# Performance work log

Measured on AMD Instinct MI355X. Metric: run time of the kernel, lower is better.

## Reference

```python
import jax, jax.numpy as jnp
import numpy as np

HEADDIM = 128
CHUNK = 256


def _ssd_scan(x, dt, A, B, C, chunk):
    # x: (b,l,h,p)  dt: (b,l,h)  A: (h,)  B,C: (b,l,n)  (single group g=1 shared by all heads)
    b, l, h, p = x.shape
    n = B.shape[-1]
    nc = l // chunk
    dA = dt * A  # (b,l,h)
    xc = x.reshape(b, nc, chunk, h, p)
    dtc = dt.reshape(b, nc, chunk, h)
    dAc = dA.reshape(b, nc, chunk, h)
    Bc = B.reshape(b, nc, chunk, n)
    Cc = C.reshape(b, nc, chunk, n)
    cs = jnp.cumsum(dAc, axis=2)  # (b,nc,c,h) cumulative log-decay within chunk
    # intra-chunk quadratic part
    CB = jnp.einsum('bjin,bjkn->bjik', Cc, Bc)  # (b,nc,c,c)
    decay = jnp.exp(cs[:, :, :, None, :] - cs[:, :, None, :, :])  # (b,nc,i,k,h)
    mask = jnp.tril(jnp.ones((chunk, chunk), dtype=bool))
    decay = jnp.where(mask[None, None, :, :, None], decay, 0.0)
    y_intra = jnp.einsum('bjik,bjikh,bjkh,bjkhp->bjihp', CB, decay, dtc, xc)
    # per-chunk end states
    decay_states = jnp.exp(cs[:, :, -1:, :] - cs)  # (b,nc,c,h)
    states = jnp.einsum('bjkh,bjkh,bjkn,bjkhp->bjhnp', decay_states, dtc, Bc, xc)
    # recurrence across chunks: h_j = exp(sum dA_j) * h_{j-1} + states_j
    chunk_decay = jnp.exp(cs[:, :, -1, :])  # (b,nc,h)
    def step(carry, inp):
        s, d = inp
        new = carry * d[:, :, None, None] + s
        return new, carry  # emit state BEFORE this chunk
    init = jnp.zeros((b, h, n, p), x.dtype)
    _, prev = jax.lax.scan(step, init,
                           (states.transpose(1, 0, 2, 3, 4), chunk_decay.transpose(1, 0, 2)))
    prev = prev.transpose(1, 0, 2, 3, 4)  # (b,nc,h,n,p)
    y_inter = jnp.einsum('bjih,bjin,bjhnp->bjihp', jnp.exp(cs), Cc, prev)
    return (y_intra + y_inter).reshape(b, l, h, p)


def setup_inputs() -> dict:
    key = jax.random.key(0)
    k1, k2, k3, k4 = jax.random.split(key, 4)
    b, l, d_inner, nheads, d_state = 2, 4096, 2048, 16, 256
    x = jax.random.normal(k1, (b, l, d_inner), dtype=jnp.float32)
    BC = jax.random.normal(k2, (b, l, 2 * d_state), dtype=jnp.float32) * 0.1
    dt = jax.random.normal(k3, (b, l, 2 * nheads), dtype=jnp.float32) - 3.0
    A_log = jnp.zeros((nheads,), dtype=jnp.float32)
    D = jnp.ones((nheads,), dtype=jnp.float32)
    W_fcD = jax.random.normal(k4, (nheads, d_inner), dtype=jnp.float32) * 0.02
    return {"x": x, "BC": BC, "dt": dt, "A_log": A_log, "D": D, "W_fcD": W_fcD}


def reference(x, BC, dt, A_log, D, W_fcD):
    b, l, dim = x.shape
    h = A_log.shape[0]
    p = HEADDIM
    d_state = BC.shape[-1] // 2
    A = -jnp.exp(A_log)
    # bidirectional: concat forward stream with time-flipped backward stream along batch
    dt2 = jnp.concatenate((dt[:, :, :h], jnp.flip(dt[:, :, h:], axis=1)), axis=0)
    dt2 = jax.nn.softplus(dt2)
    x_og = x
    x2 = jnp.concatenate((x, jnp.flip(x, axis=1)), axis=0)
    BC2 = jnp.concatenate((BC, jnp.flip(BC, axis=1)), axis=0)
    B, C = BC2[..., :d_state], BC2[..., d_state:]
    y = _ssd_scan(x2.reshape(2 * b, l, h, p), dt2, A, B, C, CHUNK)
    y = y.reshape(2 * b, l, dim)
    y = jnp.roll(y, shift=1, axis=1).at[:, 0, :].set(0.0)
    y_fw, y_bw = y[:b], jnp.flip(y[b:], axis=1)
    gate = x_og @ W_fcD.T + D  # (b,l,h)
    y = y_fw + y_bw + x_og * jnp.repeat(gate, p, axis=-1)
    return y
```

## Files before the change

kernel.cpp:

```cpp
#include <hip/hip_runtime.h>
#include <stdint.h>

#define NB 2
#define SL 4096
#define NH 16
#define HD 128
#define DS 256
#define CK 256
#define NCH 16
#define NSQ 4
#define DI 2048

typedef unsigned short u16;
typedef unsigned int u32;
typedef __attribute__((ext_vector_type(8))) __bf16 bf16x8;
typedef __attribute__((ext_vector_type(4))) float f32x4;

__device__ __forceinline__ int tor(int dir, int t) { return dir ? (SL - 1 - t) : t; }

__device__ __forceinline__ u16 f2bf(float f) {
  u32 u = __float_as_uint(f);
  u = u + 0x7fffu + ((u >> 16) & 1u);
  return (u16)(u >> 16);
}
__device__ __forceinline__ float bf2f(u16 s) {
  return __uint_as_float(((u32)s) << 16);
}

__device__ __forceinline__ void gl_lds16(const u16* g, u16* l) {
  __builtin_amdgcn_global_load_lds((const __attribute__((address_space(1))) u32*)g,
                                   (__attribute__((address_space(3))) u32*)l, 16, 0, 0);
}

__device__ __forceinline__ void stage_tile(const u16* __restrict__ src, u16* lds,
                                           int lane, int w, int k0) {
  int sgrow = lane >> 2, sc = lane & 3;
  int r0 = w << 5;
  int ra = r0 + sgrow, rb = ra + 16;
  int kqa = (sc ^ ((ra >> 1) & 3)) << 3;
  int kqb = (sc ^ ((rb >> 1) & 3)) << 3;
  gl_lds16(src + (size_t)ra * 256 + k0 + kqa, lds + r0 * 32);
  gl_lds16(src + (size_t)rb * 256 + k0 + kqb, lds + (r0 + 16) * 32);
}

__device__ __forceinline__ void stage_half(const u16* __restrict__ src, u16* lds,
                                           int lane, int w, int k0) {
  int row = (w << 4) + (lane >> 2);
  int sc = lane & 3;
  int kq = (sc ^ ((row >> 1) & 3)) << 3;
  gl_lds16(src + (size_t)row * 256 + k0 + kq, lds + (w << 4) * 32);
}

__device__ __forceinline__ bf16x8 frag(const u16* lds, int base_row, int m, int quad) {
  int row = base_row + m;
  return *(const bf16x8*)&lds[row * 32 + ((quad ^ ((row >> 1) & 3)) << 3)];
}

__device__ __forceinline__ void mfma16(const u16* As, const u16* Bs, int wi, int wp,
                                       int m, int quad, f32x4 acc[4][4]) {
  bf16x8 af[4], bv[4];
#pragma unroll
  for (int r = 0; r < 4; ++r) af[r] = frag(As, wi + (r << 4), m, quad);
#pragma unroll
  for (int c = 0; c < 4; ++c) bv[c] = frag(Bs, wp + (c << 4), m, quad);
#pragma unroll
  for (int r = 0; r < 4; ++r)
#pragma unroll
    for (int c = 0; c < 4; ++c)
      acc[r][c] = __builtin_amdgcn_mfma_f32_16x16x32_bf16(af[r], bv[c], acc[r][c], 0, 0, 0);
}

__global__ __launch_bounds__(256) void kprep(const float* __restrict__ dt,
                                             const float* __restrict__ A_log,
                                             float* __restrict__ csb,
                                             float* __restrict__ dtvb,
                                             float* __restrict__ cdecb) {
  int blk = blockIdx.x;
  int h = blk & 15, sj = blk >> 4;
  int s = sj >> 4, j = sj & 15;
  int b = s & 1, dir = s >> 1;
  int i = threadIdx.x;
  int to = tor(dir, j * CK + i);
  __shared__ float sbuf[CK];
  float a = -expf(A_log[h]);
  float raw = dt[((size_t)(b * SL + to)) * (2 * NH) + dir * NH + h];
  float sp = (raw > 20.f) ? raw : log1pf(expf(raw));
  sbuf[i] = sp * a;
  __syncthreads();
  for (int off = 1; off < CK; off <<= 1) {
    float v = (i >= off) ? sbuf[i - off] : 0.f;
    __syncthreads();
    sbuf[i] += v;
    __syncthreads();
  }
  float csv = sbuf[i];
  size_t base = ((size_t)sj * NH + h) * CK;
  csb[base + i] = csv;
  dtvb[base + i] = sp;
  if (i == CK - 1) cdecb[sj * NH + h] = expf(csv);
}

__global__ __launch_bounds__(256) void kcast(const float* __restrict__ BC,
                                             u16* __restrict__ Bbf,
                                             u16* __restrict__ Cbf) {
  int blk = blockIdx.x;
  int s = blk >> 9, tg = blk & 511;
  int b = s & 1, dir = s >> 1;
  int tid = threadIdx.x;
  int rr = tid >> 6, q = tid & 63;
  int isC = q >> 5, qq = q & 31;
#pragma unroll
  for (int it = 0; it < 2; ++it) {
    int t = tg * 8 + it * 4 + rr;
    int tsrc = tor(dir, t);
    const float* src = BC + ((size_t)(b * SL + tsrc)) * (2 * DS) + q * 8;
    float4 v0 = ((const float4*)src)[0];
    float4 v1 = ((const float4*)src)[1];
    uint4 wv;
    wv.x = (u32)f2bf(v0.x) | ((u32)f2bf(v0.y) << 16);
    wv.y = (u32)f2bf(v0.z) | ((u32)f2bf(v0.w) << 16);
    wv.z = (u32)f2bf(v1.x) | ((u32)f2bf(v1.y) << 16);
    wv.w = (u32)f2bf(v1.z) | ((u32)f2bf(v1.w) << 16);
    u16* dstb = (isC ? Cbf : Bbf) + ((size_t)s * SL + t) * DS + qq * 8;
    *(uint4*)dstb = wv;
  }
}

__global__ __launch_bounds__(256) void ktransB(const u16* __restrict__ Bbf,
                                               u16* __restrict__ BbfT) {
  int blk = blockIdx.x;
  int kslice = blk & 3, sj = blk >> 2;
  int k0 = kslice << 6;
  int s = sj >> 4, j = sj & 15;
  __shared__ u16 T[64 * 264];
  int tid = threadIdx.x;
  const u16* src = Bbf + ((size_t)s * SL + j * CK) * DS;
  u16* dst = BbfT + (size_t)sj * DS * CK;
  int kr = tid >> 2, part = (tid & 3) * 64;
  {
    const uint4* gs = (const uint4*)(src + (size_t)(k0 + kr) * DS + part);
    uint4* tb = (uint4*)&T[kr * 264 + part];
#pragma unroll
    for (int q = 0; q < 8; ++q) tb[q] = gs[q];
  }
  __syncthreads();
  int n = tid;
  u16 col[64];
#pragma unroll
  for (int kq = 0; kq < 64; ++kq) col[kq] = T[kq * 264 + n];
  uint4* ds_ = (uint4*)(dst + (size_t)n * CK + k0);
#pragma unroll
  for (int q = 0; q < 8; ++q) {
    uint4 wv;
    wv.x = (u32)col[q * 8 + 0] | ((u32)col[q * 8 + 1] << 16);
    wv.y = (u32)col[q * 8 + 2] | ((u32)col[q * 8 + 3] << 16);
    wv.z = (u32)col[q * 8 + 4] | ((u32)col[q * 8 + 5] << 16);
    wv.w = (u32)col[q * 8 + 6] | ((u32)col[q * 8 + 7] << 16);
    ds_[q] = wv;
  }
}

__global__ __launch_bounds__(256) void kxsT(const float* __restrict__ xg,
                                            const float* __restrict__ csb,
                                            const float* __restrict__ dtvb,
                                            u16* __restrict__ xsT) {
  int inst = blockIdx.x;
  int h = inst & 15, sj = inst >> 4;
  int s = sj >> 4, j = sj & 15;
  int b = s & 1, dir = s >> 1;
  int tid = threadIdx.x;
  __shared__ u16 Ls[128 * 40];
  size_t cbase = ((size_t)sj * NH + h) * CK;
  u16* dst = xsT + (size_t)inst * (128 * 256);
  int kk = tid >> 3;
  int pg = (tid & 7) * 16;
  int p2 = tid >> 1, half = tid & 1;
  for (int k0 = 0; k0 < CK; k0 += 32) {
    int kglob = k0 + kk;
    float sc_ = expf(-csb[cbase + kglob]) * dtvb[cbase + kglob];
    int t = tor(dir, j * CK + kglob);
    const float* src = xg + ((size_t)(b * SL + t)) * DI + h * HD + pg;
    float4 v0 = ((const float4*)src)[0];
    float4 v1 = ((const float4*)src)[1];
    float4 v2 = ((const float4*)src)[2];
    float4 v3 = ((const float4*)src)[3];
    float vv[16] = {v0.x, v0.y, v0.z, v0.w, v1.x, v1.y, v1.z, v1.w,
                    v2.x, v2.y, v2.z, v2.w, v3.x, v3.y, v3.z, v3.w};
    __syncthreads();
#pragma unroll
    for (int q = 0; q < 16; ++q) Ls[(pg + q) * 40 + kk] = f2bf(vv[q] * sc_);
    __syncthreads();
    uint4 w0 = *(const uint4*)&Ls[p2 * 40 + half * 16];
    uint4 w1 = *(const uint4*)&Ls[p2 * 40 + half * 16 + 8];
    *(uint4*)&dst[(size_t)p2 * 256 + k0 + half * 16] = w0;
    *(uint4*)&dst[(size_t)p2 * 256 + k0 + half * 16 + 8] = w1;
  }
}

__global__ __launch_bounds__(256) void kcb(const u16* __restrict__ Cbf,
                                           const u16* __restrict__ Bbf,
                                           u16* __restrict__ CBm) {
  int blk = blockIdx.x;
  int tri = blk % 3;
  int sj = blk / 3;
  int it0 = tri ? 128 : 0;
  int kt0 = (tri == 2) ? 128 : 0;
  int s = sj >> 4, j = sj & 15;
  __shared__ u16 As[2][128 * 32];
  __shared__ u16 Bs[2][128 * 32];
  int tid = threadIdx.x;
  int w = tid >> 6, lane = tid & 63;
  int wi = (w >> 1) << 6, wp = (w & 1) << 6;
  int m = lane & 15, quad = lane >> 4;
  const u16* Ab = Cbf + ((size_t)s * SL + j * CK + it0) * DS;
  const u16* Bb = Bbf + ((size_t)s * SL + j * CK + kt0) * DS;
  f32x4 zini = {0.f, 0.f, 0.f, 0.f};
  f32x4 acc[4][4];
#pragma unroll
  for (int r = 0; r < 4; ++r)
#pragma unroll
    for (int c = 0; c < 4; ++c) acc[r][c] = zini;
  stage_tile(Ab, As[0], lane, w, 0);
  stage_tile(Bb, Bs[0], lane, w, 0);
  __syncthreads();
  int cur = 0;
  for (int ks = 0; ks < 8; ++ks) {
    if (ks + 1 < 8) {
      int k1 = (ks + 1) << 5;
      stage_tile(Ab, As[cur ^ 1], lane, w, k1);
      stage_tile(Bb, Bs[cur ^ 1], lane, w, k1);
    }
    mfma16(As[cur], Bs[cur], wi, wp, m, quad, acc);
    __syncthreads();
    cur ^= 1;
  }
  int diag = (it0 == kt0);
  u16* dst = CBm + ((size_t)sj * CK + it0) * CK + kt0;
#pragma unroll
  for (int r = 0; r < 4; ++r)
#pragma unroll
    for (int rg = 0; rg < 4; ++rg) {
      int irow = wi + (r << 4) + (quad << 2) + rg;
#pragma unroll
      for (int c = 0; c < 4; ++c) {
        int kcol = wp + (c << 4) + m;
        float v = acc[r][c][rg];
        if (diag && kcol > irow) v = 0.f;
        dst[(size_t)irow * CK + kcol] = f2bf(v);
      }
    }
}

__global__ __launch_bounds__(512) void kstates(const u16* __restrict__ xsT,
                                               const u16* __restrict__ BbfT,
                                               const float* __restrict__ cdecb,
                                               u16* __restrict__ prevT) {
  int inst = blockIdx.x;
  int h = inst & 15, sj = inst >> 4;
  __shared__ u16 As[128 * 32];
  __shared__ u16 Bs[256 * 32];
  int tid = threadIdx.x;
  int w = tid >> 6, lane = tid & 63;
  int wi = (w >> 2) << 6;
  int wp = (w & 3) << 6;
  int m = lane & 15, quad = lane >> 4;
  const u16* Ab = xsT + (size_t)inst * (128 * 256);
  const u16* Bb = BbfT + (size_t)sj * DS * CK;
  f32x4 zini = {0.f, 0.f, 0.f, 0.f};
  f32x4 acc[4][4];
#pragma unroll
  for (int r = 0; r < 4; ++r)
#pragma unroll
    for (int c = 0; c < 4; ++c) acc[r][c] = zini;
  for (int ks = 0; ks < 8; ++ks) {
    int k0 = ks << 5;
    stage_half(Ab, As, lane, w, k0);
    stage_tile(Bb, Bs, lane, w, k0);
    __syncthreads();
    mfma16(As, Bs, wi, wp, m, quad, acc);
    __syncthreads();
  }
  float scale = cdecb[sj * NH + h];
  u16* dst = prevT + (size_t)inst * (128 * 256);
#pragma unroll
  for (int r = 0; r < 4; ++r)
#pragma unroll
    for (int rg = 0; rg < 4; ++rg) {
      int prow = wi + (r << 4) + (quad << 2) + rg;
#pragma unroll
      for (int c = 0; c < 4; ++c) {
        int ncol = wp + (c << 4) + m;
        dst[(size_t)prow * 256 + ncol] = f2bf(acc[r][c][rg] * scale);
      }
    }
}

__global__ __launch_bounds__(256) void kscan(u16* __restrict__ prevT,
                                             const float* __restrict__ cdecb) {
  int g = blockIdx.x * 256 + threadIdx.x;
  int n = g & 255;
  int p = (g >> 8) & 127;
  int h = (g >> 15) & 15;
  int s = g >> 19;
  size_t base = (((size_t)(s * 256 + h) * 128) + p) * 256 + n;
  const size_t stride = (size_t)NH * 128 * 256;
  float carry = 0.f;
  for (int j = 0; j < NCH; ++j) {
    size_t idx = base + (size_t)j * stride;
    float sv = bf2f(prevT[idx]);
    prevT[idx] = f2bf(carry);
    carry = carry * cdecb[(s * NCH + j) * NH + h] + sv;
  }
}

__global__ __launch_bounds__(512) void ky(const u16* __restrict__ CBm,
                                          const u16* __restrict__ Cbf,
                                          const u16* __restrict__ xsT,
                                          const u16* __restrict__ prevT,
                                          const float* __restrict__ csb,
                                          u16* __restrict__ ytmpb) {
  int inst = blockIdx.x;
  int h = inst & 15, sj = inst >> 4;
  int s = sj >> 4, j = sj & 15;
  __shared__ u16 As[256 * 32];
  __shared__ u16 Bs[128 * 32];
  int tid = threadIdx.x;
  int w = tid >> 6, lane = tid & 63;
  int wi = (w >> 1) << 6;
  int wp = (w & 1) << 6;
  int m = lane & 15, quad = lane >> 4;

  const u16* Ai = CBm + (size_t)sj * CK * CK;
  const u16* Ae = Cbf + ((size_t)s * SL + j * CK) * DS;
  const u16* Bi = xsT + (size_t)inst * (128 * 256);
  const u16* Be = prevT + (size_t)inst * (128 * 256);

  f32x4 zini = {0.f, 0.f, 0.f, 0.f};
  f32x4 acc[4][4];
#pragma unroll
  for (int r = 0; r < 4; ++r)
#pragma unroll
    for (int c = 0; c < 4; ++c) acc[r][c] = zini;

  for (int ks = 0; ks < 16; ++ks) {
    int intra = ks < 8;
    int k0 = (intra ? ks : ks - 8) << 5;
    if (intra) {
      if (ks < 4 || w >= 4) stage_tile(Ai, As, lane, w, k0);
    } else {
      stage_tile(Ae, As, lane, w, k0);
    }
    stage_half(intra ? Bi : Be, Bs, lane, w, k0);
    __syncthreads();
    if (!intra || ks < 4 || wi >= 128)
      mfma16(As, Bs, wi, wp, m, quad, acc);
    __syncthreads();
  }
  const float* csrow = csb + ((size_t)sj * NH + h) * CK;
  u16* yb = ytmpb + ((size_t)s * SL + j * CK) * DI + h * HD;
#pragma unroll
  for (int r = 0; r < 4; ++r)
#pragma unroll
    for (int rg = 0; rg < 4; ++rg) {
      int irow = wi + (r << 4) + (quad << 2) + rg;
      float esc = expf(csrow[irow]);
#pragma unroll
      for (int c = 0; c < 4; ++c) {
        int pcol = wp + (c << 4) + m;
        yb[(size_t)irow * DI + pcol] = f2bf(acc[r][c][rg] * esc);
      }
    }
}

__global__ __launch_bounds__(256) void kgate(const float* __restrict__ xg,
                                             const float* __restrict__ Wg,
                                             const float* __restrict__ Dg,
                                             float* __restrict__ gates) {
  int bid = blockIdx.x;
  int b = bid >> 8;
  int t0 = (bid & 255) << 4;
  __shared__ float Wl[16 * 256];
  int tid = threadIdx.x;
  int w = tid >> 6, lane = tid & 63;
  int c4 = lane << 2;

  float acc[4][16];
#pragma unroll
  for (int r = 0; r < 4; ++r)
#pragma unroll
    for (int h = 0; h < 16; ++h) acc[r][h] = 0.f;

  for (int i = 0; i < 8; ++i) {
    __syncthreads();
#pragma unroll
    for (int q = 0; q < 4; ++q) {
      int idx = q * 256 + tid;
      int h = idx >> 6;
      int c = (idx & 63) << 2;
      *(float4*)&Wl[h * 256 + c] = *(const float4*)&Wg[(size_t)h * DI + i * 256 + c];
    }
    __syncthreads();
    float4 Wf[16];
#pragma unroll
    for (int h = 0; h < 16; ++h) Wf[h] = *(const float4*)&Wl[h * 256 + c4];
#pragma unroll
    for (int r = 0; r < 4; ++r) {
      int t = t0 + (w << 2) + r;
      float4 xv = *(const float4*)&xg[((size_t)(b * SL + t)) * DI + i * 256 + c4];
#pragma unroll
      for (int h = 0; h < 16; ++h)
        acc[r][h] += xv.x * Wf[h].x + xv.y * Wf[h].y + xv.z * Wf[h].z + xv.w * Wf[h].w;
    }
  }
#pragma unroll
  for (int r = 0; r < 4; ++r)
#pragma unroll
    for (int h = 0; h < 16; ++h) {
      float v = acc[r][h];
      v += __shfl_xor(v, 32);
      v += __shfl_xor(v, 16);
      v += __shfl_xor(v, 8);
      v += __shfl_xor(v, 4);
      v += __shfl_xor(v, 2);
      v += __shfl_xor(v, 1);
      acc[r][h] = v;
    }
  if (lane == 0) {
#pragma unroll
    for (int r = 0; r < 4; ++r) {
      int t = t0 + (w << 2) + r;
      float* gdst = gates + ((size_t)(b * SL + t)) * NH;
#pragma unroll
      for (int h = 0; h < 16; ++h) gdst[h] = acc[r][h] + Dg[h];
    }
  }
}

__device__ __forceinline__ void unpk8(uint4 u, float* o) {
  o[0] = __uint_as_float(u.x << 16); o[1] = __uint_as_float(u.x & 0xffff0000u);
  o[2] = __uint_as_float(u.y << 16); o[3] = __uint_as_float(u.y & 0xffff0000u);
  o[4] = __uint_as_float(u.z << 16); o[5] = __uint_as_float(u.z & 0xffff0000u);
  o[6] = __uint_as_float(u.w << 16); o[7] = __uint_as_float(u.w & 0xffff0000u);
}

__global__ __launch_bounds__(256) void kstream(const float* __restrict__ xg,
                                               const float* __restrict__ gates,
                                               const u16* __restrict__ ytmpb,
                                               float* __restrict__ out) {
  int bid = blockIdx.x;
  int b = bid >> 10;
  int t0 = (bid & 1023) << 2;
  int tid = threadIdx.x;
  int d0 = tid << 3;
  int h8 = tid >> 4;
  const u16* fwbase = ytmpb + (size_t)b * SL * DI + d0;
  const u16* bwbase = ytmpb + (size_t)(2 + b) * SL * DI + d0;
#pragma unroll
  for (int r = 0; r < 4; ++r) {
    int t = t0 + r;
    size_t rowb = ((size_t)(b * SL + t)) * DI + d0;
    float4 x0 = *(const float4*)&xg[rowb];
    float4 x1 = *(const float4*)&xg[rowb + 4];
    float fy[8] = {0.f, 0.f, 0.f, 0.f, 0.f, 0.f, 0.f, 0.f};
    float by[8] = {0.f, 0.f, 0.f, 0.f, 0.f, 0.f, 0.f, 0.f};
    if (t > 0) unpk8(*(const uint4*)(fwbase + (size_t)(t - 1) * DI), fy);
    if (t < SL - 1) unpk8(*(const uint4*)(bwbase + (size_t)(SL - 2 - t) * DI), by);
    float g = gates[((size_t)(b * SL + t)) * NH + h8];
    float4 o0, o1;
    o0.x = fy[0] + by[0] + x0.x * g;
    o0.y = fy[1] + by[1] + x0.y * g;
    o0.z = fy[2] + by[2] + x0.z * g;
    o0.w = fy[3] + by[3] + x0.w * g;
    o1.x = fy[4] + by[4] + x1.x * g;
    o1.y = fy[5] + by[5] + x1.y * g;
    o1.z = fy[6] + by[6] + x1.z * g;
    o1.w = fy[7] + by[7] + x1.w * g;
    *(float4*)&out[rowb] = o0;
    *(float4*)&out[rowb + 4] = o1;
  }
}

extern "C" void kernel_launch(void* const* d_in, const int* in_sizes, int n_in,
                              void* d_out, int out_size, void* d_ws, size_t ws_size,
                              hipStream_t stream) {
  (void)in_sizes; (void)n_in; (void)out_size; (void)ws_size;
  const float* x     = (const float*)d_in[0];
  const float* BC    = (const float*)d_in[1];
  const float* dt    = (const float*)d_in[2];
  const float* A_log = (const float*)d_in[3];
  const float* Dg    = (const float*)d_in[4];
  const float* W     = (const float*)d_in[5];
  float* out = (float*)d_out;

  char* p = (char*)d_ws;
  float* cs    = (float*)p; p += (size_t)NSQ * NCH * NH * CK * 4;
  float* dtv   = (float*)p; p += (size_t)NSQ * NCH * NH * CK * 4;
  float* cdec  = (float*)p; p += (size_t)NSQ * NCH * NH * 4;
  float* gates = (float*)p; p += (size_t)NB * SL * NH * 4;
  u16* Bbf    = (u16*)p;    p += (size_t)NSQ * SL * DS * 2;
  u16* Cbf    = (u16*)p;    p += (size_t)NSQ * SL * DS * 2;
  u16* BbfT   = (u16*)p;    p += (size_t)NSQ * NCH * DS * CK * 2;
  u16* CBm    = (u16*)p;    p += (size_t)NSQ * NCH * CK * CK * 2;
  u16* xsT    = (u16*)p;    p += (size_t)NSQ * NCH * NH * HD * CK * 2;
  u16* prevT  = (u16*)p;    p += (size_t)NSQ * NCH * NH * HD * DS * 2;
  u16* ytmpb  = (u16*)p;    p += (size_t)NSQ * SL * DI * 2;

  hipLaunchKernelGGL(kgate,   dim3(NB * SL / 16),        dim3(256), 0, stream, x, W, Dg, gates);
  hipLaunchKernelGGL(kprep,   dim3(NSQ * NCH * NH),      dim3(CK),  0, stream, dt, A_log, cs, dtv, cdec);
  hipLaunchKernelGGL(kcast,   dim3(NSQ * SL / 8),        dim3(256), 0, stream, BC, Bbf, Cbf);
  hipLaunchKernelGGL(ktransB, dim3(NSQ * NCH * 4),       dim3(256), 0, stream, Bbf, BbfT);
  hipLaunchKernelGGL(kxsT,    dim3(NSQ * NCH * NH),      dim3(256), 0, stream, x, cs, dtv, xsT);
  hipLaunchKernelGGL(kcb,     dim3(NSQ * NCH * 3),       dim3(256), 0, stream, Cbf, Bbf, CBm);
  hipLaunchKernelGGL(kstates, dim3(NSQ * NCH * NH),      dim3(512), 0, stream, xsT, BbfT, cdec, prevT);
  hipLaunchKernelGGL(kscan,   dim3(NSQ * NH * HD * DS / 256), dim3(256), 0, stream, prevT, cdec);
  hipLaunchKernelGGL(ky,      dim3(NSQ * NCH * NH),      dim3(512), 0, stream, CBm, Cbf, xsT, prevT, cs, ytmpb);
  hipLaunchKernelGGL(kstream, dim3(NB * SL / 4),         dim3(256), 0, stream, x, gates, ytmpb, out);
}
```

Before: 383.1 us.

## Double-buffer LDS staging in GEMM kernels with explicit vmcnt waits

Converts the kstates and ky GEMM loops to double-buffered LDS staging, so the next k-slice's global-to-LDS loads are issued before computing the current one. The CB kernel's __syncthreads are replaced with explicit s_waitcnt vmcnt counts plus raw s_barrier, with scheduling barriers around them. This is meant to overlap memory latency with MFMA work. In exchange it doubles LDS usage, which can lower occupancy, and in ky it now always stages the intra-chunk CB tile rows that were previously skipped.

```diff
diff --git a/kernel.cpp b/kernel.cpp
--- a/kernel.cpp
+++ b/kernel.cpp
@@ -31,6 +31,9 @@
   __builtin_amdgcn_global_load_lds((const __attribute__((address_space(1))) u32*)g,
                                    (__attribute__((address_space(3))) u32*)l, 16, 0, 0);
 }
+
+__device__ __forceinline__ void cfence() { asm volatile("" ::: "memory"); }
+__device__ __forceinline__ void spin() { __builtin_amdgcn_sched_barrier(0); }
 
 __device__ __forceinline__ void stage_tile(const u16* __restrict__ src, u16* lds,
                                            int lane, int w, int k0) {
@@ -222,16 +225,25 @@
     for (int c = 0; c < 4; ++c) acc[r][c] = zini;
   stage_tile(Ab, As[0], lane, w, 0);
   stage_tile(Bb, Bs[0], lane, w, 0);
-  __syncthreads();
   int cur = 0;
   for (int ks = 0; ks < 8; ++ks) {
     if (ks + 1 < 8) {
       int k1 = (ks + 1) << 5;
       stage_tile(Ab, As[cur ^ 1], lane, w, k1);
       stage_tile(Bb, Bs[cur ^ 1], lane, w, k1);
-    }
+      cfence();
+      asm volatile("s_waitcnt vmcnt(4)" ::: "memory");
+    } else {
+      cfence();
+      asm volatile("s_waitcnt vmcnt(0)" ::: "memory");
+    }
+    spin();
+    __builtin_amdgcn_s_barrier();
+    spin();
     mfma16(As[cur], Bs[cur], wi, wp, m, quad, acc);
-    __syncthreads();
+    spin();
+    __builtin_amdgcn_s_barrier();
+    spin();
     cur ^= 1;
   }
   int diag = (it0 == kt0);
@@ -257,8 +269,8 @@
                                                u16* __restrict__ prevT) {
   int inst = blockIdx.x;
   int h = inst & 15, sj = inst >> 4;
-  __shared__ u16 As[128 * 32];
-  __shared__ u16 Bs[256 * 32];
+  __shared__ u16 As[2][128 * 32];
+  __shared__ u16 Bs[2][256 * 32];
   int tid = threadIdx.x;
   int w = tid >> 6, lane = tid & 63;
   int wi = (w >> 2) << 6;
@@ -272,13 +284,28 @@
   for (int r = 0; r < 4; ++r)
 #pragma unroll
     for (int c = 0; c < 4; ++c) acc[r][c] = zini;
+  stage_half(Ab, As[0], lane, w, 0);
+  stage_tile(Bb, Bs[0], lane, w, 0);
+  int cur = 0;
   for (int ks = 0; ks < 8; ++ks) {
-    int k0 = ks << 5;
-    stage_half(Ab, As, lane, w, k0);
-    stage_tile(Bb, Bs, lane, w, k0);
-    __syncthreads();
-    mfma16(As, Bs, wi, wp, m, quad, acc);
-    __syncthreads();
+    if (ks + 1 < 8) {
+      int k1 = (ks + 1) << 5;
+      stage_half(Ab, As[cur ^ 1], lane, w, k1);
+      stage_tile(Bb, Bs[cur ^ 1], lane, w, k1);
+      cfence();
+      asm volatile("s_waitcnt vmcnt(3)" ::: "memory");
+    } else {
+      cfence();
+      asm volatile("s_waitcnt vmcnt(0)" ::: "memory");
+    }
+    spin();
+    __builtin_amdgcn_s_barrier();
+    spin();
+    mfma16(As[cur], Bs[cur], wi, wp, m, quad, acc);
+    spin();
+    __builtin_amdgcn_s_barrier();
+    spin();
+    cur ^= 1;
   }
   float scale = cdecb[sj * NH + h];
   u16* dst = prevT + (size_t)inst * (128 * 256);
@@ -322,8 +349,8 @@
   int inst = blockIdx.x;
   int h = inst & 15, sj = inst >> 4;
   int s = sj >> 4, j = sj & 15;
-  __shared__ u16 As[256 * 32];
-  __shared__ u16 Bs[128 * 32];
+  __shared__ u16 As[2][256 * 32];
+  __shared__ u16 Bs[2][128 * 32];
   int tid = threadIdx.x;
   int w = tid >> 6, lane = tid & 63;
   int wi = (w >> 1) << 6;
@@ -342,19 +369,31 @@
 #pragma unroll
     for (int c = 0; c < 4; ++c) acc[r][c] = zini;
 
+  stage_tile(Ai, As[0], lane, w, 0);
+  stage_half(Bi, Bs[0], lane, w, 0);
+  int cur = 0;
   for (int ks = 0; ks < 16; ++ks) {
-    int intra = ks < 8;
-    int k0 = (intra ? ks : ks - 8) << 5;
-    if (intra) {
-      if (ks < 4 || w >= 4) stage_tile(Ai, As, lane, w, k0);
+    if (ks + 1 < 16) {
+      int ksn = ks + 1;
+      int intran = ksn < 8;
+      int k1 = (intran ? ksn : ksn - 8) << 5;
+      stage_tile(intran ? Ai : Ae, As[cur ^ 1], lane, w, k1);
+      stage_half(intran ? Bi : Be, Bs[cur ^ 1], lane, w, k1);
+      cfence();
+      asm volatile("s_waitcnt vmcnt(3)" ::: "memory");
     } else {
-      stage_tile(Ae, As, lane, w, k0);
-    }
-    stage_half(intra ? Bi : Be, Bs, lane, w, k0);
-    __syncthreads();
-    if (!intra || ks < 4 || wi >= 128)
-      mfma16(As, Bs, wi, wp, m, quad, acc);
-    __syncthreads();
+      cfence();
+      asm volatile("s_waitcnt vmcnt(0)" ::: "memory");
+    }
+    spin();
+    __builtin_amdgcn_s_barrier();
+    spin();
+    if (ks >= 8 || ks < 4 || wi >= 128)
+      mfma16(As[cur], Bs[cur], wi, wp, m, quad, acc);
+    spin();
+    __builtin_amdgcn_s_barrier();
+    spin();
+    cur ^= 1;
   }
   const float* csrow = csb + ((size_t)sj * NH + h) * CK;
   u16* yb = ytmpb + ((size_t)s * SL + j * CK) * DI + h * HD;
```

After: 361.0 us. 1.06x faster.
